# Performance work log

Measured on AMD Instinct MI355X. Metric: run time of the kernel, lower is better.

The kernel has to match this reference:

```python
import jax, jax.numpy as jnp
import numpy as np
from jax import lax

R = 128            # grid resolution (full-depth N3Tree equivalent)
BASIS = 9          # SH degree 2 -> 9 basis functions
DATA_DIM = 3 * BASIS + 1
B = 262144         # rays (512x512 image)
STEP_SIZE = 0.001
BG = 1.0           # background_brightness
NUM_STEPS = 256    # >= sqrt(3)*R worst-case voxel crossings

SH_C0 = 0.28209479177387814
SH_C1 = 0.4886025119029199
SH_C2 = (1.0925484305920792, -1.0925484305920792, 0.31539156525252005,
         -1.0925484305920792, 0.5462742152960396)


def eval_sh_bases(d):
    # d: [B,3] unit view directions -> [B,9] SH deg-2 basis values (matches svox.sh)
    x, y, z = d[:, 0], d[:, 1], d[:, 2]
    return jnp.stack([
        jnp.full_like(x, SH_C0),
        -SH_C1 * y,
        SH_C1 * z,
        -SH_C1 * x,
        SH_C2[0] * x * y,
        SH_C2[1] * y * z,
        SH_C2[2] * (2.0 * z * z - x * x - y * y),
        SH_C2[3] * x * z,
        SH_C2[4] * (x * x - y * y),
    ], axis=-1)


def dda_unit(cen, invdir):
    # slab intersection of ray (cen + t*dir) with unit cube [0,1]^3
    t1 = -cen * invdir            # [B,3]
    t2 = t1 + invdir
    tmin = jnp.maximum(jnp.max(jnp.minimum(t1, t2), axis=-1), 0.0)
    tmax = jnp.minimum(jnp.min(jnp.maximum(t1, t2), axis=-1), 1e9)
    return tmin, tmax


def setup_inputs() -> dict:
    key = jax.random.key(0)
    k1, k2, k3, k4 = jax.random.split(key, 4)
    origins = jax.random.uniform(k1, (B, 3), jnp.float32, 0.05, 0.95)
    dirs = jax.random.normal(k2, (B, 3), jnp.float32)
    viewdirs = jax.random.normal(k3, (B, 3), jnp.float32)
    viewdirs = viewdirs / jnp.linalg.norm(viewdirs, axis=-1, keepdims=True)
    tree_data = jax.random.normal(k4, (R, R, R, DATA_DIM), jnp.float32) * 0.5
    invradius = jnp.ones((3,), jnp.float32)
    return {"tree_data": tree_data, "origins": origins, "dirs": dirs,
            "viewdirs": viewdirs, "invradius": invradius}


def _render(tree_data, origins, dirs, viewdirs, invradius):
    nb = origins.shape[0]
    dirs = dirs / jnp.linalg.norm(dirs, axis=-1, keepdims=True)
    sh_mult = eval_sh_bases(viewdirs)[:, None, :]          # [B,1,9]
    invdirs = 1.0 / (dirs + 1e-9)
    t0, tmax = dda_unit(origins, invdirs)
    delta_scale = jnp.linalg.norm(dirs / invradius[None], axis=-1)  # [B]
    grid = tree_data.reshape(R * R * R, DATA_DIM)
    cube_sz = 1.0 / R

    def step(carry, _):
        t, light, out, active = carry
        pos = origins + t[:, None] * dirs                  # [B,3] in tree coords
        idx = jnp.clip(jnp.floor(pos * R), 0.0, R - 1.0)
        flat = (idx[:, 0] * (R * R) + idx[:, 1] * R + idx[:, 2]).astype(jnp.int32)
        rgba = grid[flat]                                  # [B,28] voxel query
        pos_t = pos * R - idx                              # local coords in voxel
        s0, s1 = dda_unit(pos_t, invdirs)
        dt = (s1 - s0) * cube_sz + STEP_SIZE
        sigma = jax.nn.relu(rgba[:, -1])
        att = jnp.exp(-dt * sigma * delta_scale)
        weight = light * (1.0 - att)
        rgb_sh = rgba[:, :-1].reshape(-1, 3, BASIS)
        rgb = jax.nn.sigmoid(jnp.sum(sh_mult * rgb_sh, axis=-1))  # [B,3]
        am = active[:, None]
        out = out + jnp.where(am, weight[:, None] * rgb, 0.0)
        light = jnp.where(active, light * att, light)
        t = t + jnp.where(active, dt, 0.0)
        active = active & (t < tmax)
        return (t, light, out, active), None

    init = (t0, jnp.ones((nb,), jnp.float32), jnp.zeros((nb, 3), jnp.float32),
            t0 < tmax)
    (t, light, out, active), _ = lax.scan(step, init, None, length=NUM_STEPS)
    # remaining transmittance hits background (white by default)
    return out + light[:, None] * BG


def reference(tree_data, origins, dirs, viewdirs, invradius):
    return _render(tree_data, origins, dirs, viewdirs, invradius)
```

## Files before the change

### kernel.cpp

```cpp
#include <hip/hip_runtime.h>
#include <hip/hip_fp16.h>
#include <math.h>

#define GRID_R 128
#define DATA_DIM 28
#define PAD_DIM 32
#define NSEG 8
#define SEG_STEPS 32
#define STEP_SIZE 0.001f
#define BG 1.0f

typedef _Float16 h2f __attribute__((ext_vector_type(2)));

#if __has_builtin(__builtin_amdgcn_fdot2)
__device__ __forceinline__ float fdot2(h2f a, h2f b, float c) {
    return __builtin_amdgcn_fdot2(a, b, c, false);
}
#else
__device__ __forceinline__ float fdot2(h2f a, h2f b, float c) {
    return fmaf((float)a.x, (float)b.x, fmaf((float)a.y, (float)b.y, c));
}
#endif

#if __has_builtin(__builtin_amdgcn_exp2f)
__device__ __forceinline__ float fexp2(float x)    { return __builtin_amdgcn_exp2f(x); }
__device__ __forceinline__ float fexp2neg(float x) { return __builtin_amdgcn_exp2f(-x); }
#else
__device__ __forceinline__ float fexp2(float x) {
    float r; asm("v_exp_f32 %0, %1" : "=v"(r) : "v"(x)); return r;
}
__device__ __forceinline__ float fexp2neg(float x) {
    float r; asm("v_exp_f32 %0, -%1" : "=v"(r) : "v"(x)); return r;
}
#endif

#if __has_builtin(__builtin_amdgcn_rcpf)
__device__ __forceinline__ float frcp(float x) { return __builtin_amdgcn_rcpf(x); }
#else
__device__ __forceinline__ float frcp(float x) {
    float r; asm("v_rcp_f32 %0, %1" : "=v"(r) : "v"(x)); return r;
}
#endif

__device__ __forceinline__ float march_step(
    float t, float ox, float oy, float oz,
    float dx, float dy, float dz,
    float idx, float idy, float idz, int* flat)
{
    float px = (ox + t*dx) * 128.0f;
    float py = (oy + t*dy) * 128.0f;
    float pz = (oz + t*dz) * 128.0f;
    float fx = fminf(fmaxf(floorf(px), 0.0f), 127.0f);
    float fy = fminf(fmaxf(floorf(py), 0.0f), 127.0f);
    float fz = fminf(fmaxf(floorf(pz), 0.0f), 127.0f);
    float ff = fmaf(fx, 16384.0f, fmaf(fy, 128.0f, fz));
    *flat = (int)ff;
    float cx = px - fx, cy = py - fy, cz = pz - fz;
    float a1x = -cx*idx, a1y = -cy*idy, a1z = -cz*idz;
    float a2x = a1x+idx, a2y = a1y+idy, a2z = a1z+idz;
    float e1 = fminf(fminf(fmaxf(a1x,a2x), fmaxf(a1y,a2y)), fmaxf(a1z,a2z));
    e1 = fminf(e1, 1e9f);
    return e1 * (1.0f/128.0f) + STEP_SIZE;
}

#define RAY_SETUP(i)                                                          \
    float ox = origins[3*(i)+0], oy = origins[3*(i)+1], oz = origins[3*(i)+2];\
    float dx = dirs_in[3*(i)+0], dy = dirs_in[3*(i)+1], dz = dirs_in[3*(i)+2];\
    float dn = sqrtf(dx*dx + dy*dy + dz*dz);                                  \
    float rdn = 1.0f / dn;                                                    \
    dx *= rdn; dy *= rdn; dz *= rdn;                                          \
    float idx = 1.0f / (dx + 1e-9f);                                          \
    float idy = 1.0f / (dy + 1e-9f);                                          \
    float idz = 1.0f / (dz + 1e-9f);                                          \
    float t1x = -ox*idx, t1y = -oy*idy, t1z = -oz*idz;                        \
    float t2x = t1x+idx, t2y = t1y+idy, t2z = t1z+idz;                        \
    float t0   = fmaxf(fmaxf(fmaxf(fminf(t1x,t2x), fminf(t1y,t2y)), fminf(t1z,t2z)), 0.0f); \
    float tmax = fminf(fminf(fminf(fmaxf(t1x,t2x), fmaxf(t1y,t2y)), fmaxf(t1z,t2z)), 1e9f);

__global__ __launch_bounds__(256) void prep_kernel(
    const float* __restrict__ tree, __half* __restrict__ vox, int nvox,
    const float* __restrict__ origins, const float* __restrict__ dirs_in,
    float* __restrict__ ckpt, int nB, int nGeomB)
{
    if ((int)blockIdx.x < nGeomB) {
        int i = blockIdx.x * 256 + threadIdx.x;
        if (i >= nB) return;
        RAY_SETUP(i);
        float ck[NSEG];
        float t = t0;
        ck[0] = t0;
#pragma unroll
        for (int k = 1; k < NSEG; ++k) {
            if (t < tmax) {
                for (int j = 0; j < SEG_STEPS; ++j) {
                    int fl;
                    t += march_step(t, ox, oy, oz, dx, dy, dz, idx, idy, idz, &fl);
                    if (t >= tmax) break;
                }
            }
            ck[k] = t;
        }
        float* cp = ckpt + (size_t)i * NSEG;
        *(float4*)(cp + 0) = make_float4(ck[0], ck[1], ck[2], ck[3]);
        *(float4*)(cp + 4) = make_float4(ck[4], ck[5], ck[6], ck[7]);
    } else {
        int tid2 = (blockIdx.x - nGeomB) * 256 + threadIdx.x;
        int v = tid2 >> 1;
        int q = tid2 & 1;
        if (v >= nvox) return;
        const float* src = tree + (size_t)v * DATA_DIM;
        uint4* d = (uint4*)(vox + (size_t)v * PAD_DIM) + q * 2;
        union Q { __half2 h[4]; uint4 u; } w;
        if (q == 0) {
            float4 L0 = *(const float4*)(src + 0);
            float4 L1 = *(const float4*)(src + 4);
            float4 L2 = *(const float4*)(src + 8);
            float4 L3 = *(const float4*)(src + 12);
            w.h[0] = __floats2half2_rn(L0.x, L0.y);
            w.h[1] = __floats2half2_rn(L0.z, L0.w);
            w.h[2] = __floats2half2_rn(L1.x, L1.y);
            w.h[3] = __floats2half2_rn(L1.z, L1.w);
            d[0] = w.u;
            w.h[0] = __floats2half2_rn(L2.x, 0.f);
            w.h[1] = __floats2half2_rn(L2.y, L2.z);
            w.h[2] = __floats2half2_rn(L2.w, L3.x);
            w.h[3] = __floats2half2_rn(L3.y, L3.z);
            d[1] = w.u;
        } else {
            float4 M0 = *(const float4*)(src + 12);
            float4 M1 = *(const float4*)(src + 16);
            float4 M2 = *(const float4*)(src + 20);
            float4 M3 = *(const float4*)(src + 24);
            w.h[0] = __floats2half2_rn(M0.w, M1.x);
            w.h[1] = __floats2half2_rn(M1.y, 0.f);
            w.h[2] = __floats2half2_rn(M1.z, M1.w);
            w.h[3] = __floats2half2_rn(M2.x, M2.y);
            d[0] = w.u;
            w.h[0] = __floats2half2_rn(M2.z, M2.w);
            w.h[1] = __floats2half2_rn(M3.x, M3.y);
            w.h[2] = __floats2half2_rn(M3.z, 0.f);
            w.h[3] = __floats2half2_rn(M3.w, 0.f);
            d[1] = w.u;
        }
    }
}

typedef union { uint4 u[4]; h2f h[16]; _Float16 s[32]; } Rec;

#define LOADREC(R, FLAT) do {                                                 \
    const uint4* _vp = (const uint4*)(vox_grid + (size_t)(FLAT) * PAD_DIM);   \
    (R).u[0] = _vp[0]; (R).u[1] = _vp[1];                                     \
    (R).u[2] = _vp[2]; (R).u[3] = _vp[3]; } while (0)

#define SHADE(R, DT) do {                                                     \
    float _sig = fmaxf((float)(R).s[30], 0.0f);                               \
    float _att = fexp2((DT) * _sig * nds);                                    \
    float _la  = light * _att;                                                \
    float _w   = light - _la;                                                 \
    light = _la;                                                              \
    float _r0 = fdot2((R).h[ 4], S8z, fdot2((R).h[ 3], S67, fdot2((R).h[ 2], S45, \
                fdot2((R).h[ 1], S23, fdot2((R).h[ 0], S01, 0.0f)))));        \
    float _r1 = fdot2((R).h[ 9], S8z, fdot2((R).h[ 8], S67, fdot2((R).h[ 7], S45, \
                fdot2((R).h[ 6], S23, fdot2((R).h[ 5], S01, 0.0f)))));        \
    float _r2 = fdot2((R).h[14], S8z, fdot2((R).h[13], S67, fdot2((R).h[12], S45, \
                fdot2((R).h[11], S23, fdot2((R).h[10], S01, 0.0f)))));        \
    float _g0 = frcp(1.0f + fexp2neg(_r0));                                   \
    float _g1 = frcp(1.0f + fexp2neg(_r1));                                   \
    float _g2 = frcp(1.0f + fexp2neg(_r2));                                   \
    o0 = fmaf(_w, _g0, o0);                                                   \
    o1 = fmaf(_w, _g1, o1);                                                   \
    o2 = fmaf(_w, _g2, o2); } while (0)

__global__ __launch_bounds__(256, 8) void march_kernel(
    const __half* __restrict__ vox_grid,
    const float* __restrict__ origins,
    const float* __restrict__ dirs_in,
    const float* __restrict__ viewdirs,
    const float* __restrict__ invradius,
    const float* __restrict__ ckpt,
    float* __restrict__ out, int nB)
{
    int tid = blockIdx.x * blockDim.x + threadIdx.x;
    int ray = tid >> 3;
    int seg = tid & 7;
    if (ray >= nB) return;

    RAY_SETUP(ray);

    float vx = viewdirs[3*ray+0], vy = viewdirs[3*ray+1], vz = viewdirs[3*ray+2];
    float irx = invradius[0], iry = invradius[1], irz = invradius[2];
    float qx = dx / irx, qy = dy / iry, qz = dz / irz;
    float delta_scale = sqrtf(qx*qx + qy*qy + qz*qz);

    const float C1 = 0.4886025119029199f;
    const float L2E = 1.4426950408889634f;
    float sh0 = 0.28209479177387814f;
    float sh1 = -C1 * vy;
    float sh2 =  C1 * vz;
    float sh3 = -C1 * vx;
    float sh4 =  1.0925484305920792f  * vx * vy;
    float sh5 = -1.0925484305920792f * vy * vz;
    float sh6 =  0.31539156525252005f * (2.0f*vz*vz - vx*vx - vy*vy);
    float sh7 = -1.0925484305920792f * vx * vz;
    float sh8 =  0.5462742152960396f  * (vx*vx - vy*vy);

    h2f S01 = { (_Float16)(sh0*L2E), (_Float16)(sh1*L2E) };
    h2f S23 = { (_Float16)(sh2*L2E), (_Float16)(sh3*L2E) };
    h2f S45 = { (_Float16)(sh4*L2E), (_Float16)(sh5*L2E) };
    h2f S67 = { (_Float16)(sh6*L2E), (_Float16)(sh7*L2E) };
    h2f S8z = { (_Float16)(sh8*L2E), (_Float16)0.0f      };
    float nds = -delta_scale * L2E;

    float t = ckpt[(size_t)ray * NSEG + seg];
    float light = 1.0f;
    float o0 = 0.f, o1 = 0.f, o2 = 0.f;

    if (t < tmax) {
        int fA, fB;
        Rec A, B;
        float dtA = march_step(t, ox, oy, oz, dx, dy, dz, idx, idy, idz, &fA);
        LOADREC(A, fA);
        int i = 0;
        for (;;) {
            t += dtA;
            float dtB = march_step(t, ox, oy, oz, dx, dy, dz, idx, idy, idz, &fB);
            LOADREC(B, fB);
            SHADE(A, dtA);
            if (++i >= SEG_STEPS || t >= tmax) break;

            t += dtB;
            dtA = march_step(t, ox, oy, oz, dx, dy, dz, idx, idy, idz, &fA);
            LOADREC(A, fA);
            SHADE(B, dtB);
            if (++i >= SEG_STEPS || t >= tmax) break;
        }
    }

    float l0 = __shfl(light, 0, 8);
    float l1 = __shfl(light, 1, 8);
    float l2 = __shfl(light, 2, 8);
    float l3 = __shfl(light, 3, 8);
    float l4 = __shfl(light, 4, 8);
    float l5 = __shfl(light, 5, 8);
    float l6 = __shfl(light, 6, 8);
    float l7 = __shfl(light, 7, 8);

    float P = 1.0f;
    if (seg > 0) P *= l0;
    if (seg > 1) P *= l1;
    if (seg > 2) P *= l2;
    if (seg > 3) P *= l3;
    if (seg > 4) P *= l4;
    if (seg > 5) P *= l5;
    if (seg > 6) P *= l6;
    float total_light = l0*l1*l2*l3*l4*l5*l6*l7;

    o0 *= P; o1 *= P; o2 *= P;
    o0 += __shfl_xor(o0, 1, 8); o0 += __shfl_xor(o0, 2, 8); o0 += __shfl_xor(o0, 4, 8);
    o1 += __shfl_xor(o1, 1, 8); o1 += __shfl_xor(o1, 2, 8); o1 += __shfl_xor(o1, 4, 8);
    o2 += __shfl_xor(o2, 1, 8); o2 += __shfl_xor(o2, 2, 8); o2 += __shfl_xor(o2, 4, 8);

    if (seg == 0) {
        out[3*ray+0] = o0 + total_light * BG;
        out[3*ray+1] = o1 + total_light * BG;
        out[3*ray+2] = o2 + total_light * BG;
    }
}

extern "C" void kernel_launch(void* const* d_in, const int* in_sizes, int n_in,
                              void* d_out, int out_size, void* d_ws, size_t ws_size,
                              hipStream_t stream) {
    const float* tree      = (const float*)d_in[0];
    const float* origins   = (const float*)d_in[1];
    const float* dirs      = (const float*)d_in[2];
    const float* viewdirs  = (const float*)d_in[3];
    const float* invradius = (const float*)d_in[4];
    float* out = (float*)d_out;

    int nB   = in_sizes[1] / 3;
    int nvox = in_sizes[0] / DATA_DIM;

    const int block = 256;
    __half* hgrid = (__half*)d_ws;
    float* ckpt = (float*)((char*)d_ws + (size_t)nvox * PAD_DIM * sizeof(__half));

    int nGeomB = (nB + block - 1) / block;
    int nConvB = (nvox * 2 + block - 1) / block;
    prep_kernel<<<nGeomB + nConvB, block, 0, stream>>>(
        tree, hgrid, nvox, origins, dirs, ckpt, nB, nGeomB);

    int nmarch = nB * NSEG;
    march_kernel<<<(nmarch + block - 1) / block, block, 0, stream>>>(
        hgrid, origins, dirs, viewdirs, invradius, ckpt, out, nB);
    (void)ws_size;
}
```

Baseline: 706.4 us.

## Skip shading of empty voxels via occupancy bitmask, drop software pipelining

Builds a per-voxel occupancy bitmask (sigma > 0) in the prep kernel and has the march loop test it before loading and shading a voxel record. Empty voxels contribute nothing, so their 64-byte record fetch and SH/sigmoid math are skipped. In exchange the A/B double-buffered prefetch of the next voxel is replaced by a simple loop. That adds a dependent byte load and a divergent branch on every step, which with random data (about half the voxels occupied) may cost more latency than the skipped work saves.

```diff
diff --git a/kernel.cpp b/kernel.cpp
--- a/kernel.cpp
+++ b/kernel.cpp
@@ -80,10 +80,12 @@
 __global__ __launch_bounds__(256) void prep_kernel(
     const float* __restrict__ tree, __half* __restrict__ vox, int nvox,
     const float* __restrict__ origins, const float* __restrict__ dirs_in,
-    float* __restrict__ ckpt, int nB, int nGeomB)
+    float* __restrict__ ckpt, unsigned char* __restrict__ occ_mask,
+    int nB, int nGeomB, int nConvB)
 {
-    if ((int)blockIdx.x < nGeomB) {
-        int i = blockIdx.x * 256 + threadIdx.x;
+    int bid = (int)blockIdx.x;
+    if (bid < nGeomB) {
+        int i = bid * 256 + threadIdx.x;
         if (i >= nB) return;
         RAY_SETUP(i);
         float ck[NSEG];
@@ -103,8 +105,8 @@
         float* cp = ckpt + (size_t)i * NSEG;
         *(float4*)(cp + 0) = make_float4(ck[0], ck[1], ck[2], ck[3]);
         *(float4*)(cp + 4) = make_float4(ck[4], ck[5], ck[6], ck[7]);
-    } else {
-        int tid2 = (blockIdx.x - nGeomB) * 256 + threadIdx.x;
+    } else if (bid < nGeomB + nConvB) {
+        int tid2 = (bid - nGeomB) * 256 + threadIdx.x;
         int v = tid2 >> 1;
         int q = tid2 & 1;
         if (v >= nvox) return;
@@ -142,37 +144,24 @@
             w.h[3] = __floats2half2_rn(M3.w, 0.f);
             d[1] = w.u;
         }
+    } else {
+        int m = (bid - nGeomB - nConvB) * 256 + threadIdx.x;
+        int nm = nvox >> 3;
+        if (m >= nm) return;
+        const float* s = tree + (size_t)m * 8 * DATA_DIM + (DATA_DIM - 1);
+        unsigned int b = 0;
+#pragma unroll
+        for (int j = 0; j < 8; ++j)
+            if (s[(size_t)j * DATA_DIM] > 0.0f) b |= (1u << j);
+        occ_mask[m] = (unsigned char)b;
     }
 }
 
 typedef union { uint4 u[4]; h2f h[16]; _Float16 s[32]; } Rec;
-
-#define LOADREC(R, FLAT) do {                                                 \
-    const uint4* _vp = (const uint4*)(vox_grid + (size_t)(FLAT) * PAD_DIM);   \
-    (R).u[0] = _vp[0]; (R).u[1] = _vp[1];                                     \
-    (R).u[2] = _vp[2]; (R).u[3] = _vp[3]; } while (0)
-
-#define SHADE(R, DT) do {                                                     \
-    float _sig = fmaxf((float)(R).s[30], 0.0f);                               \
-    float _att = fexp2((DT) * _sig * nds);                                    \
-    float _la  = light * _att;                                                \
-    float _w   = light - _la;                                                 \
-    light = _la;                                                              \
-    float _r0 = fdot2((R).h[ 4], S8z, fdot2((R).h[ 3], S67, fdot2((R).h[ 2], S45, \
-                fdot2((R).h[ 1], S23, fdot2((R).h[ 0], S01, 0.0f)))));        \
-    float _r1 = fdot2((R).h[ 9], S8z, fdot2((R).h[ 8], S67, fdot2((R).h[ 7], S45, \
-                fdot2((R).h[ 6], S23, fdot2((R).h[ 5], S01, 0.0f)))));        \
-    float _r2 = fdot2((R).h[14], S8z, fdot2((R).h[13], S67, fdot2((R).h[12], S45, \
-                fdot2((R).h[11], S23, fdot2((R).h[10], S01, 0.0f)))));        \
-    float _g0 = frcp(1.0f + fexp2neg(_r0));                                   \
-    float _g1 = frcp(1.0f + fexp2neg(_r1));                                   \
-    float _g2 = frcp(1.0f + fexp2neg(_r2));                                   \
-    o0 = fmaf(_w, _g0, o0);                                                   \
-    o1 = fmaf(_w, _g1, o1);                                                   \
-    o2 = fmaf(_w, _g2, o2); } while (0)
 
 __global__ __launch_bounds__(256, 8) void march_kernel(
     const __half* __restrict__ vox_grid,
+    const unsigned char* __restrict__ occ_mask,
     const float* __restrict__ origins,
     const float* __restrict__ dirs_in,
     const float* __restrict__ viewdirs,
@@ -215,25 +204,43 @@
     float light = 1.0f;
     float o0 = 0.f, o1 = 0.f, o2 = 0.f;
 
-    if (t < tmax) {
-        int fA, fB;
-        Rec A, B;
-        float dtA = march_step(t, ox, oy, oz, dx, dy, dz, idx, idy, idz, &fA);
-        LOADREC(A, fA);
-        int i = 0;
-        for (;;) {
-            t += dtA;
-            float dtB = march_step(t, ox, oy, oz, dx, dy, dz, idx, idy, idz, &fB);
-            LOADREC(B, fB);
-            SHADE(A, dtA);
-            if (++i >= SEG_STEPS || t >= tmax) break;
-
-            t += dtB;
-            dtA = march_step(t, ox, oy, oz, dx, dy, dz, idx, idy, idz, &fA);
-            LOADREC(A, fA);
-            SHADE(B, dtB);
-            if (++i >= SEG_STEPS || t >= tmax) break;
+    for (int j = 0; j < SEG_STEPS; ++j) {
+        if (t >= tmax) break;
+        int flat;
+        float dt = march_step(t, ox, oy, oz, dx, dy, dz, idx, idy, idz, &flat);
+
+        unsigned int mb = occ_mask[flat >> 3];
+        if (mb & (1u << (flat & 7))) {
+            const uint4* vp = (const uint4*)(vox_grid + (size_t)flat * PAD_DIM);
+            Rec rec;
+            rec.u[0] = vp[0]; rec.u[1] = vp[1];
+            rec.u[2] = vp[2]; rec.u[3] = vp[3];
+
+            float sigma = (float)rec.s[30];
+            float att = fexp2(dt * sigma * nds);
+            float la  = light * att;
+            float w   = light - la;
+            light = la;
+
+            float r0 = fdot2(rec.h[ 4], S8z, fdot2(rec.h[ 3], S67,
+                       fdot2(rec.h[ 2], S45, fdot2(rec.h[ 1], S23,
+                       fdot2(rec.h[ 0], S01, 0.0f)))));
+            float r1 = fdot2(rec.h[ 9], S8z, fdot2(rec.h[ 8], S67,
+                       fdot2(rec.h[ 7], S45, fdot2(rec.h[ 6], S23,
+                       fdot2(rec.h[ 5], S01, 0.0f)))));
+            float r2 = fdot2(rec.h[14], S8z, fdot2(rec.h[13], S67,
+                       fdot2(rec.h[12], S45, fdot2(rec.h[11], S23,
+                       fdot2(rec.h[10], S01, 0.0f)))));
+
+            float g0 = frcp(1.0f + fexp2neg(r0));
+            float g1 = frcp(1.0f + fexp2neg(r1));
+            float g2 = frcp(1.0f + fexp2neg(r2));
+
+            o0 = fmaf(w, g0, o0);
+            o1 = fmaf(w, g1, o1);
+            o2 = fmaf(w, g2, o2);
         }
+        t += dt;
     }
 
     float l0 = __shfl(light, 0, 8);
@@ -283,14 +290,17 @@
     const int block = 256;
     __half* hgrid = (__half*)d_ws;
     float* ckpt = (float*)((char*)d_ws + (size_t)nvox * PAD_DIM * sizeof(__half));
+    unsigned char* occ_mask =
+        (unsigned char*)((char*)ckpt + (size_t)nB * NSEG * sizeof(float));
 
     int nGeomB = (nB + block - 1) / block;
     int nConvB = (nvox * 2 + block - 1) / block;
-    prep_kernel<<<nGeomB + nConvB, block, 0, stream>>>(
-        tree, hgrid, nvox, origins, dirs, ckpt, nB, nGeomB);
+    int nMaskB = ((nvox >> 3) + block - 1) / block;
+    prep_kernel<<<nGeomB + nConvB + nMaskB, block, 0, stream>>>(
+        tree, hgrid, nvox, origins, dirs, ckpt, occ_mask, nB, nGeomB, nConvB);
 
     int nmarch = nB * NSEG;
     march_kernel<<<(nmarch + block - 1) / block, block, 0, stream>>>(
-        hgrid, origins, dirs, viewdirs, invradius, ckpt, out, nB);
+        hgrid, occ_mask, origins, dirs, viewdirs, invradius, ckpt, out, nB);
     (void)ws_size;
 }
```

Measured after the change: 641.5 us. 9.2% less time.
